# Optimization experiments

Measured on AMD Instinct MI355X. Metric: run time of the kernel, lower is better.

## Reference

```python
import jax, jax.numpy as jnp
import numpy as np

B, S, F_IN, D, H, L, E, DFF, OUT = 16, 512, 46, 256, 8, 6, 8, 1024, 3


def _ln(x, s, b, eps=1e-5):
    m = x.mean(-1, keepdims=True)
    v = ((x - m) ** 2).mean(-1, keepdims=True)
    return (x - m) / jnp.sqrt(v + eps) * s + b


def _mha(q_in, kv_in, qkv_w, qkv_b, out_w, out_b, h):
    # torch nn.MultiheadAttention (batch_first), eval mode (no dropout)
    d = q_in.shape[-1]
    dh = d // h
    wq, wk, wv = jnp.split(qkv_w, 3, axis=0)
    bq, bk, bv = jnp.split(qkv_b, 3)
    q = (q_in @ wq.T + bq).reshape(q_in.shape[0], q_in.shape[1], h, dh)
    k = (kv_in @ wk.T + bk).reshape(kv_in.shape[0], kv_in.shape[1], h, dh)
    v = (kv_in @ wv.T + bv).reshape(kv_in.shape[0], kv_in.shape[1], h, dh)
    attn = jax.nn.softmax(jnp.einsum('bqhd,bkhd->bhqk', q, k) / jnp.sqrt(jnp.float32(dh)), axis=-1)
    o = jnp.einsum('bhqk,bkhd->bqhd', attn, v).reshape(q_in.shape[0], q_in.shape[1], d)
    return o @ out_w.T + out_b


def _moe(x, gate_w, gate_b, e_w1, e_b1, e_w2, e_b2, top_k=2):
    # Faithful to source: EVERY expert runs its dense FFN over all tokens,
    # then outputs are mixed by the top-k gate weights (zero for unrouted experts).
    logits = x @ gate_w.T + gate_b                      # (B,S,E)
    tk_logits, tk_idx = jax.lax.top_k(logits, top_k)    # (B,S,K)
    tk_probs = jax.nn.softmax(tk_logits, axis=-1)
    onehot = jax.nn.one_hot(tk_idx, logits.shape[-1], dtype=x.dtype)  # (B,S,K,E)
    weights = (onehot * tk_probs[..., None]).sum(-2)    # (B,S,E)
    hid = jax.nn.gelu(jnp.einsum('bsd,efd->bsef', x, e_w1) + e_b1, approximate=False)  # (B,S,E,DFF)
    out_e = jnp.einsum('bsef,edf->bsed', hid, e_w2) + e_b2                             # (B,S,E,D)
    out = jnp.einsum('bsed,bse->bsd', out_e, weights)
    probs = jax.nn.softmax(logits, axis=-1)
    aux = logits.shape[-1] * jnp.sum(probs.mean(axis=(0, 1)) ** 2)
    return out, aux


def _posenc(s, d):
    pos = jnp.arange(s, dtype=jnp.float32)[:, None]
    div = jnp.exp(jnp.arange(0, d, 2, dtype=jnp.float32) * (-np.log(10000.0) / d))
    pe = jnp.zeros((s, d), jnp.float32)
    pe = pe.at[:, 0::2].set(jnp.sin(pos * div)).at[:, 1::2].set(jnp.cos(pos * div))
    return pe


def _forward(x, in_w, in_b, l_qkv_w, l_qkv_b, l_out_w, l_out_b, gate_w, gate_b,
             e_w1, e_b1, e_w2, e_b2, ln1_s, ln1_b, ln2_s, ln2_b,
             p_qkv_w, p_qkv_b, p_out_w, p_out_b,
             a_w1, a_b1, a_ln1s, a_ln1b, a_w2, a_b2, a_ln2s, a_ln2b, a_w3, a_b3,
             pr_w1, pr_b1, pr_ln1s, pr_ln1b, pr_w2, pr_b2, pr_ln2s, pr_ln2b, pr_w3, pr_b3):
    h = x @ in_w.T + in_b + _posenc(x.shape[1], D)[None]
    aux_total = jnp.float32(0.0)
    # NB: source builds ModuleList([encoder_layer]*L) with the SAME instance -> shared weights
    for _ in range(L):
        attn = _mha(h, h, l_qkv_w, l_qkv_b, l_out_w, l_out_b, H)
        h = _ln(h + attn, ln1_s, ln1_b)
        moe_out, aux = _moe(h, gate_w, gate_b, e_w1, e_b1, e_w2, e_b2)
        aux_total = aux_total + aux
        h = _ln(h + moe_out, ln2_s, ln2_b)
    pooled = _mha(h[:, -1:, :], h, p_qkv_w, p_qkv_b, p_out_w, p_out_b, H)[:, 0]  # (B,D)
    # action head: Linear -> GELU -> LN -> Linear -> GELU -> LN -> Linear
    a = jax.nn.gelu(pooled @ a_w1.T + a_b1, approximate=False)
    a = _ln(a, a_ln1s, a_ln1b)
    a = jax.nn.gelu(a @ a_w2.T + a_b2, approximate=False)
    a = _ln(a, a_ln2s, a_ln2b)
    action = a @ a_w3.T + a_b3
    # profit head: Linear -> LN -> GELU -> Linear -> LN -> GELU -> Linear
    p = jax.nn.gelu(_ln(pooled @ pr_w1.T + pr_b1, pr_ln1s, pr_ln1b), approximate=False)
    p = jax.nn.gelu(_ln(p @ pr_w2.T + pr_b2, pr_ln2s, pr_ln2b), approximate=False)
    profit = p @ pr_w3.T + pr_b3
    return action, profit, aux_total


def setup_inputs() -> dict:
    key = jax.random.key(0)
    ks = iter(jax.random.split(key, 64))
    def w(shape, scale=0.02):
        return jax.random.normal(next(ks), shape, jnp.float32) * scale
    d2, d4 = D // 2, D // 4
    return dict(
        x=jax.random.normal(next(ks), (B, S, F_IN), jnp.float32),
        in_w=w((D, F_IN)), in_b=jnp.zeros(D),
        l_qkv_w=w((3 * D, D)), l_qkv_b=jnp.zeros(3 * D), l_out_w=w((D, D)), l_out_b=jnp.zeros(D),
        gate_w=w((E, D)), gate_b=jnp.zeros(E),
        e_w1=w((E, DFF, D)), e_b1=jnp.zeros((E, DFF)), e_w2=w((E, D, DFF)), e_b2=jnp.zeros((E, D)),
        ln1_s=jnp.ones(D), ln1_b=jnp.zeros(D), ln2_s=jnp.ones(D), ln2_b=jnp.zeros(D),
        p_qkv_w=w((3 * D, D)), p_qkv_b=jnp.zeros(3 * D), p_out_w=w((D, D)), p_out_b=jnp.zeros(D),
        a_w1=w((d2, D)), a_b1=jnp.zeros(d2), a_ln1s=jnp.ones(d2), a_ln1b=jnp.zeros(d2),
        a_w2=w((d4, d2)), a_b2=jnp.zeros(d4), a_ln2s=jnp.ones(d4), a_ln2b=jnp.zeros(d4),
        a_w3=w((OUT, d4)), a_b3=jnp.zeros(OUT),
        pr_w1=w((D, D)), pr_b1=jnp.zeros(D), pr_ln1s=jnp.ones(D), pr_ln1b=jnp.zeros(D),
        pr_w2=w((d2, D)), pr_b2=jnp.zeros(d2), pr_ln2s=jnp.ones(d2), pr_ln2b=jnp.zeros(d2),
        pr_w3=w((1, d2)), pr_b3=jnp.zeros(1),
    )


def reference(x, in_w, in_b, l_qkv_w, l_qkv_b, l_out_w, l_out_b, gate_w, gate_b,
              e_w1, e_b1, e_w2, e_b2, ln1_s, ln1_b, ln2_s, ln2_b,
              p_qkv_w, p_qkv_b, p_out_w, p_out_b,
              a_w1, a_b1, a_ln1s, a_ln1b, a_w2, a_b2, a_ln2s, a_ln2b, a_w3, a_b3,
              pr_w1, pr_b1, pr_ln1s, pr_ln1b, pr_w2, pr_b2, pr_ln2s, pr_ln2b, pr_w3, pr_b3):
    return _forward(x, in_w, in_b, l_qkv_w, l_qkv_b, l_out_w, l_out_b, gate_w, gate_b,
                    e_w1, e_b1, e_w2, e_b2, ln1_s, ln1_b, ln2_s, ln2_b,
                    p_qkv_w, p_qkv_b, p_out_w, p_out_b,
                    a_w1, a_b1, a_ln1s, a_ln1b, a_w2, a_b2, a_ln2s, a_ln2b, a_w3, a_b3,
                    pr_w1, pr_b1, pr_ln1s, pr_ln1b, pr_w2, pr_b2, pr_ln2s, pr_ln2b, pr_w3, pr_b3)
```

## Files before the change

### kernel.cpp

```cpp
#include <hip/hip_runtime.h>
#include <hip/hip_bf16.h>
#include <math.h>


typedef __bf16 bf16;
typedef __bf16 bf16x8 __attribute__((ext_vector_type(8)));
typedef __bf16 bf16x4 __attribute__((ext_vector_type(4)));
typedef float f32x4 __attribute__((ext_vector_type(4)));

#define NIN 41

#define GLOAD_LDS(g, l)                                                    \
    __builtin_amdgcn_global_load_lds(                                      \
        (const __attribute__((address_space(1))) void*)(g),                \
        (__attribute__((address_space(3))) void*)(l), 16, 0, 0)

struct InTab {
    const void* src[NIN];
    unsigned off[NIN];
    unsigned n[NIN];
};

__device__ __forceinline__ float gelu_exact(float x) {
    return 0.5f * x * (1.0f + erff(x * 0.70710678118654752f));
}

__global__ void sniff_kernel(const unsigned* __restrict__ xw, int* __restrict__ flag) {
    __shared__ int cnt;
    if (threadIdx.x == 0) cnt = 0;
    __syncthreads();
    const unsigned w = xw[threadIdx.x];
    const unsigned ex = (w >> 7) & 0xFFu;
    if (ex >= 107u && ex <= 133u) atomicAdd(&cnt, 1);
    __syncthreads();
    if (threadIdx.x == 0) *flag = (cnt >= 192) ? 1 : 0;
}

__global__ __launch_bounds__(256) void convert_kernel(
    InTab tab, bf16* __restrict__ dst_base, const int* __restrict__ flag) {
    const unsigned g0 = blockIdx.x * 1024u;
    int inp = 0;
#pragma unroll
    for (int i = 1; i < NIN; i++)
        if (g0 >= tab.off[i]) inp = i;
    const unsigned n = tab.n[inp];
    const unsigned i0 = g0 - tab.off[inp] + threadIdx.x * 4u;
    if (i0 >= n) return;
    const int isbf = *flag;
    bf16* dst = dst_base + tab.off[inp];
    const unsigned end = (i0 + 4u > n) ? n : i0 + 4u;
    if (isbf) {
        const unsigned short* s = (const unsigned short*)tab.src[inp];
        for (unsigned i = i0; i < end; i++) ((unsigned short*)dst)[i] = s[i];
    } else {
        const float* s = (const float*)tab.src[inp];
        for (unsigned i = i0; i < end; i++) dst[i] = (bf16)s[i];
    }
}

__global__ void out_convert_kernel(const float* __restrict__ st, void* __restrict__ out,
                                   const int* __restrict__ flag) {
    const int i = threadIdx.x;
    if (i >= 65) return;
    if (*flag) ((bf16*)out)[i] = (bf16)st[i];
    else       ((float*)out)[i] = st[i];
}

#define SWZ(r, c) (((r) * 8 + ((c) ^ ((r) & 7))) * 8)

template <int BM, int BN, int WM, int WN, bool VTOUT>
__global__ __launch_bounds__(256) void gemm_bt(
    const bf16* __restrict__ A, const bf16* __restrict__ W,
    const bf16* __restrict__ bias, bf16* __restrict__ C,
    int M, int N, int K, bf16* __restrict__ vT) {
    constexpr int BK = 64;
    __shared__ alignas(16) bf16 As[BM * BK];
    __shared__ alignas(16) bf16 Ws[BN * BK];
    const int bm0 = blockIdx.x * BM, bn0 = blockIdx.y * BN;
    const int tid = threadIdx.x;
    const int wave = tid >> 6, lane = tid & 63;
    constexpr int WCOLS = BN / WN;
    const int wm0 = (wave / WCOLS) * WM, wn0 = (wave % WCOLS) * WN;
    constexpr int MT = WM / 16, NT = WN / 16;
    f32x4 acc[MT][NT] = {};
    const int frow = lane & 15, fquad = lane >> 4;

    constexpr int AIT = BM / 32, BIT = BN / 32;
    const bf16* ag[AIT];
    const bf16* bg[BIT];
    unsigned al[AIT], bl[BIT];
#pragma unroll
    for (int i = 0; i < AIT; i++) {
        const int d = wave * (BM * 2) + i * 64 + lane;
        const int r = d >> 3, c = ((d & 7) ^ (r & 7)) * 8;
        ag[i] = A + (size_t)(bm0 + r) * K + c;
        al[i] = (unsigned)(wave * (BM * 2) + i * 64) * 8u;
    }
#pragma unroll
    for (int i = 0; i < BIT; i++) {
        const int d = wave * (BN * 2) + i * 64 + lane;
        const int r = d >> 3, c = ((d & 7) ^ (r & 7)) * 8;
        bg[i] = W + (size_t)(bn0 + r) * K + c;
        bl[i] = (unsigned)(wave * (BN * 2) + i * 64) * 8u;
    }

    for (int k0 = 0; k0 < K; k0 += BK) {
#pragma unroll
        for (int i = 0; i < AIT; i++) GLOAD_LDS(ag[i] + k0, &As[al[i]]);
#pragma unroll
        for (int i = 0; i < BIT; i++) GLOAD_LDS(bg[i] + k0, &Ws[bl[i]]);
        __syncthreads();
#pragma unroll
        for (int ks = 0; ks < BK / 32; ks++) {
            bf16x8 af[MT], bfr[NT];
#pragma unroll
            for (int mt = 0; mt < MT; mt++) {
                const int r = wm0 + mt * 16 + frow;
                af[mt] = *(const bf16x8*)&As[SWZ(r, ks * 4 + fquad)];
            }
#pragma unroll
            for (int nt = 0; nt < NT; nt++) {
                const int r = wn0 + nt * 16 + frow;
                bfr[nt] = *(const bf16x8*)&Ws[SWZ(r, ks * 4 + fquad)];
            }
#pragma unroll
            for (int mt = 0; mt < MT; mt++)
#pragma unroll
                for (int nt = 0; nt < NT; nt++)
                    acc[mt][nt] = __builtin_amdgcn_mfma_f32_16x16x32_bf16(
                        af[mt], bfr[nt], acc[mt][nt], 0, 0, 0);
        }
        __syncthreads();
    }

#pragma unroll
    for (int mt = 0; mt < MT; mt++)
#pragma unroll
        for (int nt = 0; nt < NT; nt++) {
            const int gn = bn0 + wn0 + nt * 16 + frow;
            const float bv = (float)bias[gn];
#pragma unroll
            for (int r = 0; r < 4; r++) {
                const int gm = bm0 + wm0 + mt * 16 + fquad * 4 + r;
                const float v = acc[mt][nt][r] + bv;
                if (VTOUT && gn >= 512) {
                    const int d = gn - 512;
                    const int bb = gm >> 9, s = gm & 511;
                    vT[((size_t)(bb * 8 + (d >> 5)) * 32 + (d & 31)) * 512 + s] = (bf16)v;
// ... 118 lines not shown
    const bf16* bg[2];
    unsigned al[4], bl[2];
#pragma unroll
    for (int i = 0; i < 4; i++) {
        const int d = wave * 256 + i * 64 + lane;
        const int r = d >> 3, c = ((d & 7) ^ (r & 7)) * 8;
        ag[i] = A + (size_t)(bm0 + r) * K + c;
        al[i] = (unsigned)(wave * 256 + i * 64) * 8u;
    }
#pragma unroll
    for (int i = 0; i < 2; i++) {
        const int d = wave * 128 + i * 64 + lane;
        const int r = d >> 3, c = ((d & 7) ^ (r & 7)) * 8;
        bg[i] = W + (size_t)(bn0 + r) * K + c;
        bl[i] = (unsigned)(wave * 128 + i * 64) * 8u;
    }

    for (int k0 = 0; k0 < K; k0 += BK) {
#pragma unroll
        for (int i = 0; i < 4; i++) GLOAD_LDS(ag[i] + k0, &As[al[i]]);
#pragma unroll
        for (int i = 0; i < 2; i++) GLOAD_LDS(bg[i] + k0, &Ws[bl[i]]);
        __syncthreads();
#pragma unroll
        for (int ks = 0; ks < 2; ks++) {
            bf16x8 af[MT], bfr[NT];
#pragma unroll
            for (int mt = 0; mt < MT; mt++) {
                const int r = wm0 + mt * 16 + frow;
                af[mt] = *(const bf16x8*)&As[SWZ(r, ks * 4 + fquad)];
            }
#pragma unroll
            for (int nt = 0; nt < NT; nt++) {
                const int r = nt * 16 + frow;
                bfr[nt] = *(const bf16x8*)&Ws[SWZ(r, ks * 4 + fquad)];
            }
#pragma unroll
            for (int mt = 0; mt < MT; mt++)
#pragma unroll
                for (int nt = 0; nt < NT; nt++)
                    acc[mt][nt] = __builtin_amdgcn_mfma_f32_16x16x32_bf16(
                        af[mt], bfr[nt], acc[mt][nt], 0, 0, 0);
        }
        __syncthreads();
    }

#pragma unroll
    for (int mt = 0; mt < MT; mt++)
#pragma unroll
        for (int nt = 0; nt < NT; nt++) {
            const int gn = bn0 + nt * 16 + frow;
            const float bv = (float)bias[gn];
#pragma unroll
            for (int r = 0; r < 4; r++) {
                const int gm = bm0 + wm0 + mt * 16 + fquad * 4 + r;
                const float v = acc[mt][nt][r] + bv;
                C[(size_t)mylist[gm] * 256 + gn] = (bf16)(mylw[gm] * v);
            }
        }
}

__global__ __launch_bounds__(256) void input_proj_kernel(
    const bf16* __restrict__ x, const bf16* __restrict__ w,
    const bf16* __restrict__ b, bf16* __restrict__ h) {
    const int m = blockIdx.x, t = threadIdx.x;
    __shared__ float xs[46];
    if (t < 46) xs[t] = (float)x[m * 46 + t];
    __syncthreads();
    float acc = (float)b[t];
#pragma unroll
    for (int k = 0; k < 46; k++) acc += xs[k] * (float)w[t * 46 + k];
    const int s = m & 511;
    const int i = t >> 1;
    const float dv = expf((float)(2 * i) * (-9.210340371976184f / 256.0f));
    const float ang = (float)s * dv;
    const float pe = (t & 1) ? cosf(ang) : sinf(ang);
    h[(size_t)m * 256 + t] = (bf16)(acc + pe);
}

__global__ __launch_bounds__(256) void ln_kernel(
    bf16* __restrict__ h, const bf16* __restrict__ a0,
    const bf16* __restrict__ a1, const bf16* __restrict__ s,
    const bf16* __restrict__ b) {
    const int m = blockIdx.x * 4 + (threadIdx.x >> 6);
    const int lane = threadIdx.x & 63;
    const int c0 = lane * 4;
    bf16x4 hv = *(const bf16x4*)&h[(size_t)m * 256 + c0];
    bf16x4 av = *(const bf16x4*)&a0[(size_t)m * 256 + c0];
    bf16x4 bv2 = *(const bf16x4*)&a1[(size_t)m * 256 + c0];
    float x[4];
    float s1 = 0.0f, s2 = 0.0f;
#pragma unroll
    for (int j = 0; j < 4; j++) {
        x[j] = (float)hv[j] + (float)av[j] + (float)bv2[j];
        s1 += x[j];
        s2 += x[j] * x[j];
    }
#pragma unroll
    for (int msk = 1; msk < 64; msk <<= 1) {
        s1 += __shfl_xor(s1, msk, 64);
        s2 += __shfl_xor(s2, msk, 64);
    }
    const float mean = s1 * (1.0f / 256.0f);
    const float var = fmaxf(s2 * (1.0f / 256.0f) - mean * mean, 0.0f);
    const float inv = rsqrtf(var + 1e-5f);
    bf16x4 sv = *(const bf16x4*)&s[c0];
    bf16x4 bv = *(const bf16x4*)&b[c0];
    bf16x4 o;
#pragma unroll
    for (int j = 0; j < 4; j++)
        o[j] = (bf16)((x[j] - mean) * inv * (float)sv[j] + (float)bv[j]);
    *(bf16x4*)&h[(size_t)m * 256 + c0] = o;
}

__global__ __launch_bounds__(256) void gate_ln_kernel(
    bf16* __restrict__ h, const bf16* __restrict__ addv,
    const bf16* __restrict__ lns, const bf16* __restrict__ lnb,
    const bf16* __restrict__ gw, const bf16* __restrict__ gb,
    int* __restrict__ top_e, float* __restrict__ top_w,
    int* __restrict__ g_hist, float* __restrict__ aux_sums) {
    __shared__ alignas(16) bf16 hs[128][264];
    __shared__ alignas(16) bf16 gws[8][264];
    __shared__ float lg[128][9];
    __shared__ float mxs[128], invs[128];
    __shared__ int hist[16];
    const int tid = threadIdx.x;
    {
        const int e = tid >> 5, k = (tid & 31) * 8;
        *(bf16x8*)&gws[e][k] = *(const bf16x8*)&gw[e * 256 + k];
    }
    if (tid < 16) hist[tid] = 0;

    const int tl = tid >> 1, half = tid & 1;
    const int tok = blockIdx.x * 128 + tl;
    const int c0 = half * 128;
    float s1 = 0.0f, s2 = 0.0f;
#pragma unroll
    for (int j = 0; j < 128; j += 8) {
        bf16x8 hv = *(const bf16x8*)&h[(size_t)tok * 256 + c0 + j];
        bf16x8 av = *(const bf16x8*)&addv[(size_t)tok * 256 + c0 + j];
        bf16x8 xw;
#pragma unroll
        for (int q = 0; q < 8; q++) {
            const float xq = (float)hv[q] + (float)av[q];
            xw[q] = (bf16)xq;
            s1 += xq;
            s2 += xq * xq;
        }
        *(bf16x8*)&hs[tl][c0 + j] = xw;
    }
    s1 += __shfl_xor(s1, 1, 64);
    s2 += __shfl_xor(s2, 1, 64);
    const float mean = s1 * (1.0f / 256.0f);
    const float var = fmaxf(s2 * (1.0f / 256.0f) - mean * mean, 0.0f);
    const float inv = rsqrtf(var + 1e-5f);
#pragma unroll
    for (int j = 0; j < 128; j += 8) {
        bf16x8 xw = *(const bf16x8*)&hs[tl][c0 + j];
        bf16x8 sv = *(const bf16x8*)&lns[c0 + j];
        bf16x8 bv = *(const bf16x8*)&lnb[c0 + j];
        bf16x8 o;
#pragma unroll
        for (int q = 0; q < 8; q++)
            o[q] = (bf16)(((float)xw[q] - mean) * inv * (float)sv[q] + (float)bv[q]);
        *(bf16x8*)&hs[tl][c0 + j] = o;
        *(bf16x8*)&h[(size_t)tok * 256 + c0 + j] = o;
    }
    __syncthreads();

    const int e = tid & 7;
#pragma unroll
    for (int pass = 0; pass < 4; pass++) {
        const int t2 = pass * 32 + (tid >> 3);
        float acc = 0.0f;
        for (int k = 0; k < 256; k += 8) {
            bf16x8 hv = *(const bf16x8*)&hs[t2][k];
            bf16x8 wv = *(const bf16x8*)&gws[e][k];
#pragma unroll
            for (int q = 0; q < 8; q++) acc += (float)hv[q] * (float)wv[q];
        }
        lg[t2][e] = acc + (float)gb[e];
    }
    __syncthreads();

    if (tid < 128) {
        const int t2 = blockIdx.x * 128 + tid;
        float l[8];
#pragma unroll
        for (int j = 0; j < 8; j++) l[j] = lg[tid][j];
        int i0 = 0;
#pragma unroll
        for (int j = 1; j < 8; j++)
            if (l[j] > l[i0]) i0 = j;
        int i1 = -1;
#pragma unroll
        for (int j = 0; j < 8; j++)
            if (j != i0 && (i1 < 0 || l[j] > l[i1])) i1 = j;
        const float p0 = 1.0f / (1.0f + expf(l[i1] - l[i0]));
        top_e[t2] = i0;         top_w[t2] = p0;
        top_e[8192 + t2] = i1;  top_w[8192 + t2] = 1.0f - p0;
        atomicAdd(&hist[i0], 1);
        atomicAdd(&hist[8 + i1], 1);
        const float mx = l[i0];
        float se = 0.0f;
#pragma unroll
        for (int j = 0; j < 8; j++) se += expf(l[j] - mx);
        mxs[tid] = mx;
        invs[tid] = 1.0f / se;
    }
    __syncthreads();
    if (tid < 8) {
        float s = 0.0f;
        for (int t = 0; t < 128; t++) s += expf(lg[t][tid] - mxs[t]) * invs[t];
        atomicAdd(&aux_sums[tid], s);
    }
    if (tid < 16) g_hist[blockIdx.x * 16 + tid] = hist[tid];
}

__global__ __launch_bounds__(256) void scatter_route_kernel(
    const int* __restrict__ g_hist, const int* __restrict__ top_e,
    const float* __restrict__ top_w, int* __restrict__ ntiles,
    int* __restrict__ tile_ex, int* __restrict__ list, float* __restrict__ lw) {
    __shared__ int gh[64][16];
    __shared__ int s_cnt[16], s_pre[16], s_off[16], pos[16];
    const int tid = threadIdx.x;
    for (int i = tid; i < 1024; i += 256) gh[i >> 4][i & 15] = g_hist[i];
    __syncthreads();
    if (tid < 16) {
        int run = 0, pre = 0;
        for (int b = 0; b < 64; b++) {
            if (b == (int)blockIdx.x) pre = run;
            run += gh[b][tid];
        }
        s_cnt[tid] = run;
        s_pre[tid] = pre;
    }
    __syncthreads();
    if (tid < 2) {
        const int slot = tid;
        int o = 0;
        for (int e2 = 0; e2 < 8; e2++) {
            s_off[slot * 8 + e2] = o;
            const int nt = (s_cnt[slot * 8 + e2] + 127) >> 7;
            if (blockIdx.x == 0)
                for (int t = 0; t < nt; t++) tile_ex[slot * 72 + (o >> 7) + t] = e2;
            o += nt << 7;
        }
        if (blockIdx.x == 0) ntiles[slot] = o >> 7;
    }
    __syncthreads();
    if (tid < 16) pos[tid] = s_off[tid] + s_pre[tid];
    __syncthreads();
    if (blockIdx.x == 0) {
        for (int idx = tid; idx < 16 * 128; idx += 256) {
            const int seg = idx >> 7, i = idx & 127;
            const int slot = seg >> 3;
            const int start = s_off[seg] + s_cnt[seg];
            const int end = s_off[seg] + ((s_cnt[seg] + 127) & ~127);
            const int p = start + i;
            if (p < end) {
                list[slot * 9216 + p] = 8192;
                lw[slot * 9216 + p] = 0.0f;
            }
        }
    }
    if (tid < 128) {
        const int tok = blockIdx.x * 128 + tid;
#pragma unroll
        for (int slot = 0; slot < 2; slot++) {
            const int e = top_e[slot * 8192 + tok];
            const float w = top_w[slot * 8192 + tok];
            const int idx = atomicAdd(&pos[slot * 8 + e], 1);
            list[slot * 9216 + idx] = tok;
            lw[slot * 9216 + idx] = w;
        }
    }
}

__global__ __launch_bounds__(256) void attn_kernel(
    const bf16* __restrict__ qkv, const bf16* __restrict__ vT,
    bf16* __restrict__ aout) {
    __shared__ alignas(16) bf16 P[32][520];
    __shared__ float wsum[4][32];
    __shared__ float sinv[32];
    const int s0 = blockIdx.x * 32;
    const int b = blockIdx.y >> 3, hh = blockIdx.y & 7;
    const int tid = threadIdx.x, wave = tid >> 6, lane = tid & 63;
    const int frow = lane & 15, fquad = lane >> 4;
    const size_t base = (size_t)b * 512;
    const float CST = 0.25505654f;

    bf16x8 qf[2];
#pragma unroll
    for (int mt = 0; mt < 2; mt++)
        qf[mt] = *(const bf16x8*)&qkv[(base + s0 + mt * 16 + frow) * 768 + hh * 32 + fquad * 8];
    float rsum[2][4] = {};
#pragma unroll
    for (int k8 = 0; k8 < 8; k8++) {
        const int key0 = (wave * 8 + k8) * 16;
        bf16x8 kf = *(const bf16x8*)&qkv[(base + key0 + frow) * 768 + 256 + hh * 32 + fquad * 8];
#pragma unroll
        for (int mt = 0; mt < 2; mt++) {
            f32x4 c = {};
            c = __builtin_amdgcn_mfma_f32_16x16x32_bf16(qf[mt], kf, c, 0, 0, 0);
#pragma unroll
            for (int r = 0; r < 4; r++) {
                const float e_ = __builtin_exp2f(fminf(c[r] * CST, 60.0f));
                P[mt * 16 + fquad * 4 + r][key0 + frow] = (bf16)e_;
                rsum[mt][r] += e_;
            }
        }
    }
#pragma unroll
    for (int mt = 0; mt < 2; mt++)
#pragma unroll
        for (int r = 0; r < 4; r++) {
#pragma unroll
            for (int m = 1; m < 16; m <<= 1)
                rsum[mt][r] += __shfl_xor(rsum[mt][r], m, 64);
        }
    if (frow == 0) {
#pragma unroll
        for (int mt = 0; mt < 2; mt++)
#pragma unroll
            for (int r = 0; r < 4; r++)
                wsum[wave][mt * 16 + fquad * 4 + r] = rsum[mt][r];
    }
    __syncthreads();
    if (tid < 32)
        sinv[tid] = 1.0f / (wsum[0][tid] + wsum[1][tid] + wsum[2][tid] + wsum[3][tid]);

    {
        const int mt = wave >> 1, nt = wave & 1;
        const bf16* vrow = &vT[((size_t)(b * 8 + hh) * 32 + nt * 16 + frow) * 512];
        f32x4 o = {};
#pragma unroll
        for (int ks = 0; ks < 16; ks++) {
            bf16x8 pf = *(const bf16x8*)&P[mt * 16 + frow][ks * 32 + fquad * 8];
            bf16x8 vf = *(const bf16x8*)&vrow[ks * 32 + fquad * 8];
            o = __builtin_amdgcn_mfma_f32_16x16x32_bf16(pf, vf, o, 0, 0, 0);
        }
        __syncthreads();
        const int r0 = mt * 16 + fquad * 4;
#pragma unroll
        for (int r = 0; r < 4; r++)
            aout[(base + s0 + r0 + r) * 256 + hh * 32 + nt * 16 + frow] =
                (bf16)(o[r] * sinv[r0 + r]);
    }
}

__global__ __launch_bounds__(256) void pooled_attn_kernel(
    const bf16* __restrict__ qkv, const bf16* __restrict__ vT,
    bf16* __restrict__ pa) {
    const int wid = blockIdx.x * 4 + (threadIdx.x >> 6);
    const int lane = threadIdx.x & 63;
    const int b = wid >> 3, hh = wid & 7;
    const size_t base = (size_t)b * 512;
    const float scale = 0.17677669529663687f;
    float q[32];
#pragma unroll
    for (int d = 0; d < 32; d++) q[d] = (float)qkv[(base + 511) * 768 + hh * 32 + d];
    float sc[8];
    float mx = -1e30f;
#pragma unroll
    for (int j = 0; j < 8; j++) {
        const int key = lane + j * 64;
        const bf16* kr = &qkv[(base + key) * 768 + 256 + hh * 32];
        float s = 0.0f;
#pragma unroll
        for (int d = 0; d < 32; d++) s += q[d] * (float)kr[d];
        s *= scale;
        sc[j] = s;
        mx = fmaxf(mx, s);
    }
#pragma unroll
    for (int m = 1; m < 64; m <<= 1) mx = fmaxf(mx, __shfl_xor(mx, m, 64));
    float se = 0.0f;
#pragma unroll
    for (int j = 0; j < 8; j++) { sc[j] = expf(sc[j] - mx); se += sc[j]; }
#pragma unroll
    for (int m = 1; m < 64; m <<= 1) se += __shfl_xor(se, m, 64);
    float o[32] = {};
    const bf16* vb = &vT[(size_t)(b * 8 + hh) * 32 * 512];
#pragma unroll
    for (int d = 0; d < 32; d++) {
        const bf16* vr = vb + (size_t)d * 512;
#pragma unroll
        for (int j = 0; j < 8; j++)
            o[d] += sc[j] * (float)vr[lane + j * 64];
    }
#pragma unroll
    for (int d = 0; d < 32; d++) {
#pragma unroll
        for (int m = 1; m < 64; m <<= 1) o[d] += __shfl_xor(o[d], m, 64);
    }
    if (lane == 0) {
        const float inv = 1.0f / se;
        for (int d = 0; d < 32; d++) pa[b * 256 + hh * 32 + d] = (bf16)(o[d] * inv);
    }
}

__global__ __launch_bounds__(256) void pooled_proj_kernel(
    const bf16* __restrict__ pa, const bf16* __restrict__ w,
    const bf16* __restrict__ bias, bf16* __restrict__ pooled) {
    const int b = blockIdx.x, t = threadIdx.x;
    __shared__ float xs[256];
    xs[t] = (float)pa[b * 256 + t];
    __syncthreads();
    float acc = (float)bias[t];
    for (int k = 0; k < 256; k++) acc += xs[k] * (float)w[t * 256 + k];
    pooled[b * 256 + t] = (bf16)acc;
}

__global__ __launch_bounds__(256) void heads_kernel(
    const bf16* __restrict__ pooled,
    const bf16* __restrict__ aw1, const bf16* __restrict__ ab1,
    const bf16* __restrict__ aln1s, const bf16* __restrict__ aln1b,
    const bf16* __restrict__ aw2, const bf16* __restrict__ ab2,
    const bf16* __restrict__ aln2s, const bf16* __restrict__ aln2b,
    const bf16* __restrict__ aw3, const bf16* __restrict__ ab3,
    const bf16* __restrict__ pw1, const bf16* __restrict__ pb1,
    const bf16* __restrict__ pln1s, const bf16* __restrict__ pln1b,
    const bf16* __restrict__ pw2, const bf16* __restrict__ pb2,
    const bf16* __restrict__ pln2s, const bf16* __restrict__ pln2b,
    const bf16* __restrict__ pw3, const bf16* __restrict__ pb3,
    float* __restrict__ out) {
    const int b = blockIdx.x, t = threadIdx.x;
    __shared__ float pool[256], buf[256], buf2[256], r1[256], r2[256];
    pool[t] = (float)pooled[b * 256 + t];
    __syncthreads();

    auto block_ln = [&](float* v, int W, const bf16* ls, const bf16* lb) {
        const float val = (t < W) ? v[t] : 0.0f;
        r1[t] = val;
        r2[t] = val * val;
        __syncthreads();
        for (int off = 128; off > 0; off >>= 1) {
            if (t < off) { r1[t] += r1[t + off]; r2[t] += r2[t + off]; }
            __syncthreads();
        }
        const float mean = r1[0] / (float)W;
        const float var = fmaxf(r2[0] / (float)W - mean * mean, 0.0f);
        const float inv = rsqrtf(var + 1e-5f);
        __syncthreads();
        if (t < W) v[t] = (val - mean) * inv * (float)ls[t] + (float)lb[t];
        __syncthreads();
    };

    float a;
    if (t < 128) {
        a = (float)ab1[t];
        for (int k = 0; k < 256; k++) a += pool[k] * (float)aw1[t * 256 + k];
        buf[t] = gelu_exact(a);
    }
    __syncthreads();
    block_ln(buf, 128, aln1s, aln1b);
    if (t < 64) {
        a = (float)ab2[t];
        for (int k = 0; k < 128; k++) a += buf[k] * (float)aw2[t * 128 + k];
        buf2[t] = gelu_exact(a);
    }
    __syncthreads();
    block_ln(buf2, 64, aln2s, aln2b);
    if (t < 3) {
        a = (float)ab3[t];
        for (int k = 0; k < 64; k++) a += buf2[k] * (float)aw3[t * 64 + k];
        out[b * 3 + t] = a;
    }

    a = (float)pb1[t];
    for (int k = 0; k < 256; k++) a += pool[k] * (float)pw1[t * 256 + k];
    buf[t] = a;
    __syncthreads();
    block_ln(buf, 256, pln1s, pln1b);
    buf[t] = gelu_exact(buf[t]);
    __syncthreads();
    if (t < 128) {
        a = (float)pb2[t];
        for (int k = 0; k < 256; k++) a += buf[k] * (float)pw2[t * 256 + k];
        buf2[t] = a;
    }
    __syncthreads();
    block_ln(buf2, 128, pln2s, pln2b);
    if (t < 128) buf2[t] = gelu_exact(buf2[t]);
    __syncthreads();
    if (t == 0) {
        a = (float)pb3[0];
        for (int k = 0; k < 128; k++) a += buf2[k] * (float)pw3[k];
        out[48 + b] = a;
    }
}

__global__ void aux_kernel(const float* __restrict__ sums, float* __restrict__ out) {
    if (threadIdx.x == 0 && blockIdx.x == 0) {
        float tot = 0.0f;
        for (int l = 0; l < 6; l++)
            for (int e = 0; e < 8; e++) {
                const float mn = sums[l * 8 + e] * (1.0f / 8192.0f);
                tot += 8.0f * mn * mn;
            }
        out[64] = tot;
    }
}

extern "C" void kernel_launch(void* const* d_in, const int* in_sizes, int n_in,
                              void* d_out, int out_size, void* d_ws, size_t ws_size,
                              hipStream_t stream) {
    char* ws = (char*)d_ws;
    const size_t MB = 1024 * 1024;
    bf16*  h     = (bf16*)(ws);
    bf16*  moe0  = (bf16*)(ws + 8 * MB);
    bf16*  moe1  = (bf16*)(ws + 13 * MB);
    char*  ctrl  = ws + 20 * MB;
    float* auxs   = (float*)(ctrl + 0);
    int*   flag   = (int*)(ctrl + 192);
    int*   ntiles = (int*)(ctrl + 256);
    int*   tileex = (int*)(ctrl + 320);
    float* ostage = (float*)(ctrl + 1024);
    int*   g_hist = (int*)(ctrl + 2048);
    int*   top_e  = (int*)(ctrl + 10240);
    float* top_w  = (float*)(ctrl + 75776);
    int*   list   = (int*)(ctrl + 141312);
    float* lw     = (float*)(ctrl + 215040);
    bf16*  qkv   = (bf16*)(ws + 24 * MB);
    bf16*  aoutb = (bf16*)(ws + 40 * MB);
    bf16*  projo = (bf16*)(ws + 48 * MB);
    bf16*  hid0  = (bf16*)(ws + 56 * MB);
    bf16*  hid1  = (bf16*)(ws + 80 * MB);
    bf16*  vT    = (bf16*)(ws + 104 * MB);
    bf16*  pattn  = (bf16*)(ws + 110 * MB);
    bf16*  pooled = (bf16*)(ws + 110 * MB + 8192);
    bf16*  cvbase = (bf16*)(ws + 112 * MB);

    InTab tab;
    unsigned off = 0;
    bf16* cv[NIN];
    for (int i = 0; i < NIN; i++) {
        tab.src[i] = d_in[i];
        tab.off[i] = off;
        tab.n[i] = (unsigned)in_sizes[i];
        cv[i] = cvbase + off;
        off += ((unsigned)in_sizes[i] + 1023u) & ~1023u;
    }
    const int cv_blocks = (int)(off >> 10);

    const bf16 *x = cv[0], *in_w = cv[1], *in_b = cv[2], *qkv_w = cv[3], *qkv_b = cv[4],
               *out_w = cv[5], *out_b = cv[6], *gate_w = cv[7], *gate_b = cv[8],
               *e_w1 = cv[9], *e_b1 = cv[10], *e_w2 = cv[11], *e_b2 = cv[12],
               *ln1_s = cv[13], *ln1_b = cv[14], *ln2_s = cv[15], *ln2_b = cv[16],
               *pqkv_w = cv[17], *pqkv_b = cv[18], *pout_w = cv[19], *pout_b = cv[20],
               *a_w1 = cv[21], *a_b1 = cv[22], *a_ln1s = cv[23], *a_ln1b = cv[24],
               *a_w2 = cv[25], *a_b2 = cv[26], *a_ln2s = cv[27], *a_ln2b = cv[28],
               *a_w3 = cv[29], *a_b3 = cv[30],
               *pr_w1 = cv[31], *pr_b1 = cv[32], *pr_ln1s = cv[33], *pr_ln1b = cv[34],
               *pr_w2 = cv[35], *pr_b2 = cv[36], *pr_ln2s = cv[37], *pr_ln2b = cv[38],
               *pr_w3 = cv[39], *pr_b3 = cv[40];

    sniff_kernel<<<1, 256, 0, stream>>>((const unsigned*)d_in[0], flag);
    convert_kernel<<<cv_blocks, 256, 0, stream>>>(tab, cvbase, flag);

    hipMemsetAsync(auxs, 0, 192, stream);
    input_proj_kernel<<<8192, 256, 0, stream>>>(x, in_w, in_b, h);

    for (int l = 0; l < 6; l++) {
        gemm_bt<64, 128, 32, 64, true><<<dim3(128, 6), 256, 0, stream>>>(
            h, qkv_w, qkv_b, qkv, 8192, 768, 256, vT);
        attn_kernel<<<dim3(16, 128), 256, 0, stream>>>(qkv, vT, aoutb);
        gemm_bt<64, 64, 32, 32, false><<<dim3(128, 4), 256, 0, stream>>>(
            aoutb, out_w, out_b, projo, 8192, 256, 256, vT);
        gate_ln_kernel<<<64, 256, 0, stream>>>(h, projo, ln1_s, ln1_b,
                                               gate_w, gate_b,
                                               top_e, top_w, g_hist, auxs + l * 8);
        scatter_route_kernel<<<64, 256, 0, stream>>>(g_hist, top_e, top_w,
                                                     ntiles, tileex, list, lw);
        gemm_moe_w1<<<dim3(142, 8), 256, 0, stream>>>(
            h, e_w1, e_b1, hid0, hid1, list, tileex, ntiles);
        gemm_moe_w2<<<dim3(142, 4), 256, 0, stream>>>(
            hid0, hid1, e_w2, e_b2, moe0, moe1, list, lw, tileex, ntiles);
        ln_kernel<<<2048, 256, 0, stream>>>(h, moe0, moe1, ln2_s, ln2_b);
    }

    gemm_bt<64, 128, 32, 64, true><<<dim3(128, 6), 256, 0, stream>>>(
        h, pqkv_w, pqkv_b, qkv, 8192, 768, 256, vT);
    pooled_attn_kernel<<<32, 256, 0, stream>>>(qkv, vT, pattn);
    pooled_proj_kernel<<<16, 256, 0, stream>>>(pattn, pout_w, pout_b, pooled);

    heads_kernel<<<16, 256, 0, stream>>>(
        pooled,
        a_w1, a_b1, a_ln1s, a_ln1b, a_w2, a_b2, a_ln2s, a_ln2b, a_w3, a_b3,
        pr_w1, pr_b1, pr_ln1s, pr_ln1b, pr_w2, pr_b2, pr_ln2s, pr_ln2b, pr_w3, pr_b3,
        ostage);
    aux_kernel<<<1, 64, 0, stream>>>(auxs, ostage);
    out_convert_kernel<<<1, 128, 0, stream>>>(ostage, d_out, flag);
}
```

Baseline: 1.090 ms.

## Fuse attention out-projection with residual LN and gating; merge pooled and head kernels

Replaces the separate out-projection GEMM and gate/LN kernel with a single kernel that does the projection, residual add, LayerNorm, gate logits, top-2 routing and aux sums for 32-row tiles. This removes the projo round trip and a launch per layer. The pooled attention, pooled projection and head MLPs become one 512-thread kernel, and the aux reduction moves into the output conversion kernel. The routing prefix scan is adapted to the larger number of histogram blocks, and the second LN kernel is widened to 8-element vectors.

After: 1.010 ms. -7.4%, faster.

```diff
diff --git a/kernel.cpp b/kernel.cpp
--- a/kernel.cpp
+++ b/kernel.cpp
@@ -58,12 +58,26 @@
     }
 }
 
-__global__ void out_convert_kernel(const float* __restrict__ st, void* __restrict__ out,
+__global__ void out_convert_kernel(const float* __restrict__ st,
+                                   const float* __restrict__ auxsums,
+                                   void* __restrict__ out,
                                    const int* __restrict__ flag) {
     const int i = threadIdx.x;
     if (i >= 65) return;
-    if (*flag) ((bf16*)out)[i] = (bf16)st[i];
-    else       ((float*)out)[i] = st[i];
+    float v;
+    if (i == 64) {
+        float tot = 0.0f;
+        for (int l = 0; l < 6; l++)
+            for (int e = 0; e < 8; e++) {
+                const float mn = auxsums[l * 8 + e] * (1.0f / 8192.0f);
+                tot += 8.0f * mn * mn;
+            }
+        v = tot;
+    } else {
+        v = st[i];
+    }
+    if (*flag) ((bf16*)out)[i] = (bf16)v;
+    else       ((float*)out)[i] = v;
 }
 
 #define SWZ(r, c) (((r) * 8 + ((c) ^ ((r) & 7))) * 8)
@@ -348,112 +362,209 @@
     bf16* __restrict__ h, const bf16* __restrict__ a0,
     const bf16* __restrict__ a1, const bf16* __restrict__ s,
     const bf16* __restrict__ b) {
-    const int m = blockIdx.x * 4 + (threadIdx.x >> 6);
-    const int lane = threadIdx.x & 63;
-    const int c0 = lane * 4;
-    bf16x4 hv = *(const bf16x4*)&h[(size_t)m * 256 + c0];
-    bf16x4 av = *(const bf16x4*)&a0[(size_t)m * 256 + c0];
-    bf16x4 bv2 = *(const bf16x4*)&a1[(size_t)m * 256 + c0];
-    float x[4];
+    const int wv = threadIdx.x >> 6, lane = threadIdx.x & 63;
+    const int m = blockIdx.x * 8 + wv * 2 + (lane >> 5);
+    const int c0 = (lane & 31) * 8;
+    const size_t off = (size_t)m * 256 + c0;
+    bf16x8 hv = *(const bf16x8*)&h[off];
+    bf16x8 av = *(const bf16x8*)&a0[off];
+    bf16x8 bv2 = *(const bf16x8*)&a1[off];
+    float x[8];
     float s1 = 0.0f, s2 = 0.0f;
 #pragma unroll
-    for (int j = 0; j < 4; j++) {
+    for (int j = 0; j < 8; j++) {
         x[j] = (float)hv[j] + (float)av[j] + (float)bv2[j];
         s1 += x[j];
         s2 += x[j] * x[j];
     }
 #pragma unroll
-    for (int msk = 1; msk < 64; msk <<= 1) {
+    for (int msk = 1; msk < 32; msk <<= 1) {
         s1 += __shfl_xor(s1, msk, 64);
         s2 += __shfl_xor(s2, msk, 64);
     }
     const float mean = s1 * (1.0f / 256.0f);
     const float var = fmaxf(s2 * (1.0f / 256.0f) - mean * mean, 0.0f);
     const float inv = rsqrtf(var + 1e-5f);
-    bf16x4 sv = *(const bf16x4*)&s[c0];
-    bf16x4 bv = *(const bf16x4*)&b[c0];
-    bf16x4 o;
-#pragma unroll
-    for (int j = 0; j < 4; j++)
+    bf16x8 sv = *(const bf16x8*)&s[c0];
+    bf16x8 bv = *(const bf16x8*)&b[c0];
+    bf16x8 o;
+#pragma unroll
+    for (int j = 0; j < 8; j++)
         o[j] = (bf16)((x[j] - mean) * inv * (float)sv[j] + (float)bv[j]);
-    *(bf16x4*)&h[(size_t)m * 256 + c0] = o;
-}
-
-__global__ __launch_bounds__(256) void gate_ln_kernel(
-    bf16* __restrict__ h, const bf16* __restrict__ addv,
+    *(bf16x8*)&h[off] = o;
+}
+
+__global__ __launch_bounds__(256) void proj_gate_ln_kernel(
+    const bf16* __restrict__ A, const bf16* __restrict__ W,
+    const bf16* __restrict__ bias, bf16* __restrict__ h,
     const bf16* __restrict__ lns, const bf16* __restrict__ lnb,
     const bf16* __restrict__ gw, const bf16* __restrict__ gb,
     int* __restrict__ top_e, float* __restrict__ top_w,
     int* __restrict__ g_hist, float* __restrict__ aux_sums) {
-    __shared__ alignas(16) bf16 hs[128][264];
-    __shared__ alignas(16) bf16 gws[8][264];
-    __shared__ float lg[128][9];
-    __shared__ float mxs[128], invs[128];
-    __shared__ int hist[16];
+    __shared__ alignas(16) bf16 As[32 * 64];
+    __shared__ alignas(16) bf16 Ws[256 * 64];
+    __shared__ alignas(16) bf16 hs[32 * 264];
+    __shared__ alignas(16) bf16 gws[8 * 264];
+    __shared__ float rws1[4][32], rws2[4][32];
+    __shared__ float meanv[32], invv[32];
+    __shared__ float lg[256];
+    __shared__ int sh_hist[16];
+    __shared__ float sh_aux[8];
+
+    const int bm0 = blockIdx.x * 32;
     const int tid = threadIdx.x;
+    const int wave = tid >> 6, lane = tid & 63;
+    const int wn0 = (wave & 3) * 64;
+    const int frow = lane & 15, fquad = lane >> 4;
+    f32x4 acc[2][4] = {};
+
+    const int da = wave * 64 + lane;
+    const int ra = da >> 3, ca = ((da & 7) ^ (ra & 7)) * 8;
+    const bf16* ag = A + (size_t)(bm0 + ra) * 256 + ca;
+    const unsigned al = (unsigned)(wave * 64) * 8u;
+    const bf16* bg[8];
+    unsigned bl[8];
+#pragma unroll
+    for (int i = 0; i < 8; i++) {
+        const int d = wave * 512 + i * 64 + lane;
+        const int r = d >> 3, c = ((d & 7) ^ (r & 7)) * 8;
+        bg[i] = W + (size_t)r * 256 + c;
+        bl[i] = (unsigned)(wave * 512 + i * 64) * 8u;
+    }
+
+    {
+        const int rr = tid >> 3, ccb = (tid & 7) * 32;
+        const bf16* src = &h[(size_t)(bm0 + rr) * 256 + ccb];
+        bf16x8 v0 = *(const bf16x8*)&src[0];
+        bf16x8 v1 = *(const bf16x8*)&src[8];
+        bf16x8 v2 = *(const bf16x8*)&src[16];
+        bf16x8 v3 = *(const bf16x8*)&src[24];
+        bf16* dst = &hs[rr * 264 + ccb];
+        *(bf16x8*)&dst[0] = v0;
+        *(bf16x8*)&dst[8] = v1;
+        *(bf16x8*)&dst[16] = v2;
+        *(bf16x8*)&dst[24] = v3;
+    }
     {
         const int e = tid >> 5, k = (tid & 31) * 8;
-        *(bf16x8*)&gws[e][k] = *(const bf16x8*)&gw[e * 256 + k];
-    }
-    if (tid < 16) hist[tid] = 0;
-
-    const int tl = tid >> 1, half = tid & 1;
-    const int tok = blockIdx.x * 128 + tl;
-    const int c0 = half * 128;
-    float s1 = 0.0f, s2 = 0.0f;
-#pragma unroll
-    for (int j = 0; j < 128; j += 8) {
-        bf16x8 hv = *(const bf16x8*)&h[(size_t)tok * 256 + c0 + j];
-        bf16x8 av = *(const bf16x8*)&addv[(size_t)tok * 256 + c0 + j];
-        bf16x8 xw;
-#pragma unroll
-        for (int q = 0; q < 8; q++) {
-            const float xq = (float)hv[q] + (float)av[q];
-            xw[q] = (bf16)xq;
-            s1 += xq;
-            s2 += xq * xq;
-        }
-        *(bf16x8*)&hs[tl][c0 + j] = xw;
-    }
-    s1 += __shfl_xor(s1, 1, 64);
-    s2 += __shfl_xor(s2, 1, 64);
-    const float mean = s1 * (1.0f / 256.0f);
-    const float var = fmaxf(s2 * (1.0f / 256.0f) - mean * mean, 0.0f);
-    const float inv = rsqrtf(var + 1e-5f);
-#pragma unroll
-    for (int j = 0; j < 128; j += 8) {
-        bf16x8 xw = *(const bf16x8*)&hs[tl][c0 + j];
-        bf16x8 sv = *(const bf16x8*)&lns[c0 + j];
-        bf16x8 bv = *(const bf16x8*)&lnb[c0 + j];
-        bf16x8 o;
-#pragma unroll
-        for (int q = 0; q < 8; q++)
-            o[q] = (bf16)(((float)xw[q] - mean) * inv * (float)sv[q] + (float)bv[q]);
-        *(bf16x8*)&hs[tl][c0 + j] = o;
-        *(bf16x8*)&h[(size_t)tok * 256 + c0 + j] = o;
-    }
-    __syncthreads();
-
-    const int e = tid & 7;
-#pragma unroll
-    for (int pass = 0; pass < 4; pass++) {
-        const int t2 = pass * 32 + (tid >> 3);
-        float acc = 0.0f;
+        *(bf16x8*)&gws[e * 264 + k] = *(const bf16x8*)&gw[e * 256 + k];
+    }
+    if (tid < 16) sh_hist[tid] = 0;
+    if (tid < 8) sh_aux[tid] = 0.0f;
+
+    for (int k0 = 0; k0 < 256; k0 += 64) {
+        GLOAD_LDS(ag + k0, &As[al]);
+#pragma unroll
+        for (int i = 0; i < 8; i++) GLOAD_LDS(bg[i] + k0, &Ws[bl[i]]);
+        __syncthreads();
+#pragma unroll
+        for (int ks = 0; ks < 2; ks++) {
+            bf16x8 af[2], bfr[4];
+#pragma unroll
+            for (int mt = 0; mt < 2; mt++)
+                af[mt] = *(const bf16x8*)&As[SWZ(mt * 16 + frow, ks * 4 + fquad)];
+#pragma unroll
+            for (int nt = 0; nt < 4; nt++)
+                bfr[nt] = *(const bf16x8*)&Ws[SWZ(wn0 + nt * 16 + frow, ks * 4 + fquad)];
+#pragma unroll
+            for (int mt = 0; mt < 2; mt++)
+#pragma unroll
+                for (int nt = 0; nt < 4; nt++)
+                    acc[mt][nt] = __builtin_amdgcn_mfma_f32_16x16x32_bf16(
+                        af[mt], bfr[nt], acc[mt][nt], 0, 0, 0);
+        }
+        __syncthreads();
+    }
+
+    float s1v[2][4] = {}, s2v[2][4] = {};
+#pragma unroll
+    for (int mt = 0; mt < 2; mt++)
+#pragma unroll
+        for (int nt = 0; nt < 4; nt++) {
+            const int gn = wn0 + nt * 16 + frow;
+            const float bv = (float)bias[gn];
+#pragma unroll
+            for (int r = 0; r < 4; r++) {
+                const int row = mt * 16 + fquad * 4 + r;
+                const float x = acc[mt][nt][r] + bv + (float)hs[row * 264 + gn];
+                acc[mt][nt][r] = x;
+                s1v[mt][r] += x;
+                s2v[mt][r] += x * x;
+            }
+        }
+#pragma unroll
+    for (int mt = 0; mt < 2; mt++)
+#pragma unroll
+        for (int r = 0; r < 4; r++) {
+#pragma unroll
+            for (int m = 1; m < 16; m <<= 1) {
+                s1v[mt][r] += __shfl_xor(s1v[mt][r], m, 64);
+                s2v[mt][r] += __shfl_xor(s2v[mt][r], m, 64);
+            }
+        }
+    if (frow == 0) {
+#pragma unroll
+        for (int mt = 0; mt < 2; mt++)
+#pragma unroll
+            for (int r = 0; r < 4; r++) {
+                const int row = mt * 16 + fquad * 4 + r;
+                rws1[wave][row] = s1v[mt][r];
+                rws2[wave][row] = s2v[mt][r];
+            }
+    }
+    __syncthreads();
+    if (tid < 32) {
+        const float a = rws1[0][tid] + rws1[1][tid] + rws1[2][tid] + rws1[3][tid];
+        const float c2 = rws2[0][tid] + rws2[1][tid] + rws2[2][tid] + rws2[3][tid];
+        const float mean = a * (1.0f / 256.0f);
+        const float var = fmaxf(c2 * (1.0f / 256.0f) - mean * mean, 0.0f);
+        meanv[tid] = mean;
+        invv[tid] = rsqrtf(var + 1e-5f);
+    }
+    __syncthreads();
+
+#pragma unroll
+    for (int mt = 0; mt < 2; mt++)
+#pragma unroll
+        for (int nt = 0; nt < 4; nt++) {
+            const int gn = wn0 + nt * 16 + frow;
+            const float sg = (float)lns[gn], bgn = (float)lnb[gn];
+#pragma unroll
+            for (int r = 0; r < 4; r++) {
+                const int row = mt * 16 + fquad * 4 + r;
+                const float o = (acc[mt][nt][r] - meanv[row]) * invv[row] * sg + bgn;
+                hs[row * 264 + gn] = (bf16)o;
+            }
+        }
+    __syncthreads();
+
+    {
+        const int rr = tid >> 3, ccb = (tid & 7) * 32;
+        bf16* dst = &h[(size_t)(bm0 + rr) * 256 + ccb];
+        const bf16* src = &hs[rr * 264 + ccb];
+        *(bf16x8*)&dst[0] = *(const bf16x8*)&src[0];
+        *(bf16x8*)&dst[8] = *(const bf16x8*)&src[8];
+        *(bf16x8*)&dst[16] = *(const bf16x8*)&src[16];
+        *(bf16x8*)&dst[24] = *(const bf16x8*)&src[24];
+    }
+    {
+        const int row = tid >> 3, e = tid & 7;
+        float acg = (float)gb[e];
         for (int k = 0; k < 256; k += 8) {
-            bf16x8 hv = *(const bf16x8*)&hs[t2][k];
-            bf16x8 wv = *(const bf16x8*)&gws[e][k];
-#pragma unroll
-            for (int q = 0; q < 8; q++) acc += (float)hv[q] * (float)wv[q];
-        }
-        lg[t2][e] = acc + (float)gb[e];
-    }
-    __syncthreads();
-
-    if (tid < 128) {
-        const int t2 = blockIdx.x * 128 + tid;
+            bf16x8 hv = *(const bf16x8*)&hs[row * 264 + k];
+            bf16x8 wv = *(const bf16x8*)&gws[e * 264 + k];
+#pragma unroll
+            for (int q = 0; q < 8; q++) acg += (float)hv[q] * (float)wv[q];
+        }
+        lg[row * 8 + e] = acg;
+    }
+    __syncthreads();
+
+    if (tid < 32) {
+        const int tok = bm0 + tid;
         float l[8];
 #pragma unroll
-        for (int j = 0; j < 8; j++) l[j] = lg[tid][j];
+        for (int j = 0; j < 8; j++) l[j] = lg[tid * 8 + j];
         int i0 = 0;
 #pragma unroll
         for (int j = 1; j < 8; j++)
@@ -463,41 +574,47 @@
         for (int j = 0; j < 8; j++)
             if (j != i0 && (i1 < 0 || l[j] > l[i1])) i1 = j;
         const float p0 = 1.0f / (1.0f + expf(l[i1] - l[i0]));
-        top_e[t2] = i0;         top_w[t2] = p0;
-        top_e[8192 + t2] = i1;  top_w[8192 + t2] = 1.0f - p0;
-        atomicAdd(&hist[i0], 1);
-        atomicAdd(&hist[8 + i1], 1);
+        top_e[tok] = i0;         top_w[tok] = p0;
+        top_e[8192 + tok] = i1;  top_w[8192 + tok] = 1.0f - p0;
+        atomicAdd(&sh_hist[i0], 1);
+        atomicAdd(&sh_hist[8 + i1], 1);
         const float mx = l[i0];
         float se = 0.0f;
 #pragma unroll
-        for (int j = 0; j < 8; j++) se += expf(l[j] - mx);
-        mxs[tid] = mx;
-        invs[tid] = 1.0f / se;
-    }
-    __syncthreads();
-    if (tid < 8) {
-        float s = 0.0f;
-        for (int t = 0; t < 128; t++) s += expf(lg[t][tid] - mxs[t]) * invs[t];
-        atomicAdd(&aux_sums[tid], s);
-    }
-    if (tid < 16) g_hist[blockIdx.x * 16 + tid] = hist[tid];
+        for (int j = 0; j < 8; j++) { l[j] = expf(l[j] - mx); se += l[j]; }
+        const float si = 1.0f / se;
+#pragma unroll
+        for (int j = 0; j < 8; j++) atomicAdd(&sh_aux[j], l[j] * si);
+    }
+    __syncthreads();
+    if (tid < 16) g_hist[blockIdx.x * 16 + tid] = sh_hist[tid];
+    if (tid < 8) atomicAdd(&aux_sums[tid], sh_aux[tid]);
 }
 
 __global__ __launch_bounds__(256) void scatter_route_kernel(
     const int* __restrict__ g_hist, const int* __restrict__ top_e,
     const float* __restrict__ top_w, int* __restrict__ ntiles,
     int* __restrict__ tile_ex, int* __restrict__ list, float* __restrict__ lw) {
-    __shared__ int gh[64][16];
+    __shared__ int gh[256][16];
+    __shared__ int ps[16][8];
     __shared__ int s_cnt[16], s_pre[16], s_off[16], pos[16];
     const int tid = threadIdx.x;
-    for (int i = tid; i < 1024; i += 256) gh[i >> 4][i & 15] = g_hist[i];
+    for (int i = tid; i < 4096; i += 256) gh[i >> 4][i & 15] = g_hist[i];
+    __syncthreads();
+    if (tid < 128) {
+        const int se = tid >> 3, ch = tid & 7;
+        int s = 0;
+        for (int b = ch * 32; b < ch * 32 + 32; b++) s += gh[b][se];
+        ps[se][ch] = s;
+    }
     __syncthreads();
     if (tid < 16) {
-        int run = 0, pre = 0;
-        for (int b = 0; b < 64; b++) {
-            if (b == (int)blockIdx.x) pre = run;
-            run += gh[b][tid];
-        }
+        int run = 0;
+        for (int ch = 0; ch < 8; ch++) run += ps[tid][ch];
+        const int b0 = (int)blockIdx.x * 4;
+        int pre = 0;
+        for (int ch = 0; ch < (b0 >> 5); ch++) pre += ps[tid][ch];
+        for (int b = b0 & ~31; b < b0; b++) pre += gh[b][tid];
         s_cnt[tid] = run;
         s_pre[tid] = pre;
     }
@@ -615,71 +732,9 @@
     }
 }
 
-__global__ __launch_bounds__(256) void pooled_attn_kernel(
+__global__ __launch_bounds__(512) void pooled_heads_kernel(
     const bf16* __restrict__ qkv, const bf16* __restrict__ vT,
-    bf16* __restrict__ pa) {
-    const int wid = blockIdx.x * 4 + (threadIdx.x >> 6);
-    const int lane = threadIdx.x & 63;
-    const int b = wid >> 3, hh = wid & 7;
-    const size_t base = (size_t)b * 512;
-    const float scale = 0.17677669529663687f;
-    float q[32];
-#pragma unroll
-    for (int d = 0; d < 32; d++) q[d] = (float)qkv[(base + 511) * 768 + hh * 32 + d];
-    float sc[8];
-    float mx = -1e30f;
-#pragma unroll
-    for (int j = 0; j < 8; j++) {
-        const int key = lane + j * 64;
-        const bf16* kr = &qkv[(base + key) * 768 + 256 + hh * 32];
-        float s = 0.0f;
-#pragma unroll
-        for (int d = 0; d < 32; d++) s += q[d] * (float)kr[d];
-        s *= scale;
-        sc[j] = s;
-        mx = fmaxf(mx, s);
-    }
-#pragma unroll
-    for (int m = 1; m < 64; m <<= 1) mx = fmaxf(mx, __shfl_xor(mx, m, 64));
-    float se = 0.0f;
-#pragma unroll
-    for (int j = 0; j < 8; j++) { sc[j] = expf(sc[j] - mx); se += sc[j]; }
-#pragma unroll
-    for (int m = 1; m < 64; m <<= 1) se += __shfl_xor(se, m, 64);
-    float o[32] = {};
-    const bf16* vb = &vT[(size_t)(b * 8 + hh) * 32 * 512];
-#pragma unroll
-    for (int d = 0; d < 32; d++) {
-        const bf16* vr = vb + (size_t)d * 512;
-#pragma unroll
-        for (int j = 0; j < 8; j++)
-            o[d] += sc[j] * (float)vr[lane + j * 64];
-    }
-#pragma unroll
-    for (int d = 0; d < 32; d++) {
-#pragma unroll
-        for (int m = 1; m < 64; m <<= 1) o[d] += __shfl_xor(o[d], m, 64);
-    }
-    if (lane == 0) {
-        const float inv = 1.0f / se;
-        for (int d = 0; d < 32; d++) pa[b * 256 + hh * 32 + d] = (bf16)(o[d] * inv);
-    }
-}
-
-__global__ __launch_bounds__(256) void pooled_proj_kernel(
-    const bf16* __restrict__ pa, const bf16* __restrict__ w,
-    const bf16* __restrict__ bias, bf16* __restrict__ pooled) {
-    const int b = blockIdx.x, t = threadIdx.x;
-    __shared__ float xs[256];
-    xs[t] = (float)pa[b * 256 + t];
-    __syncthreads();
-    float acc = (float)bias[t];
-    for (int k = 0; k < 256; k++) acc += xs[k] * (float)w[t * 256 + k];
-    pooled[b * 256 + t] = (bf16)acc;
-}
-
-__global__ __launch_bounds__(256) void heads_kernel(
-    const bf16* __restrict__ pooled,
+    const bf16* __restrict__ pout_w, const bf16* __restrict__ pout_b,
     const bf16* __restrict__ aw1, const bf16* __restrict__ ab1,
     const bf16* __restrict__ aln1s, const bf16* __restrict__ aln1b,
     const bf16* __restrict__ aw2, const bf16* __restrict__ ab2,
@@ -692,14 +747,71 @@
     const bf16* __restrict__ pw3, const bf16* __restrict__ pb3,
     float* __restrict__ out) {
     const int b = blockIdx.x, t = threadIdx.x;
+    __shared__ float pa_s[256];
     __shared__ float pool[256], buf[256], buf2[256], r1[256], r2[256];
-    pool[t] = (float)pooled[b * 256 + t];
+
+    {
+        const int hh = t >> 6, lane = t & 63;
+        const size_t base = (size_t)b * 512;
+        const float scale = 0.17677669529663687f;
+        float q[32];
+#pragma unroll
+        for (int d = 0; d < 32; d++) q[d] = (float)qkv[(base + 511) * 768 + hh * 32 + d];
+        float sc[8];
+        float mx = -1e30f;
+#pragma unroll
+        for (int j = 0; j < 8; j++) {
+            const int key = lane + j * 64;
+            const bf16* kr = &qkv[(base + key) * 768 + 256 + hh * 32];
+            float s = 0.0f;
+#pragma unroll
+            for (int d = 0; d < 32; d++) s += q[d] * (float)kr[d];
+            s *= scale;
+            sc[j] = s;
+            mx = fmaxf(mx, s);
+        }
+#pragma unroll
+        for (int m = 1; m < 64; m <<= 1) mx = fmaxf(mx, __shfl_xor(mx, m, 64));
+        float se = 0.0f;
+#pragma unroll
+        for (int j = 0; j < 8; j++) { sc[j] = expf(sc[j] - mx); se += sc[j]; }
+#pragma unroll
+        for (int m = 1; m < 64; m <<= 1) se += __shfl_xor(se, m, 64);
+        float o[32] = {};
+        const bf16* vb = &vT[(size_t)(b * 8 + hh) * 32 * 512];
+#pragma unroll
+        for (int d = 0; d < 32; d++) {
+            const bf16* vr = vb + (size_t)d * 512;
+#pragma unroll
+            for (int j = 0; j < 8; j++)
+                o[d] += sc[j] * (float)vr[lane + j * 64];
+        }
+#pragma unroll
+        for (int d = 0; d < 32; d++) {
+#pragma unroll
+            for (int m = 1; m < 64; m <<= 1) o[d] += __shfl_xor(o[d], m, 64);
+        }
+        if (lane == 0) {
+            const float inv = 1.0f / se;
+            for (int d = 0; d < 32; d++) pa_s[hh * 32 + d] = o[d] * inv;
+        }
+    }
+    __syncthreads();
+
+    if (t < 256) {
+        float a = (float)pout_b[t];
+        for (int k = 0; k < 256; k++) a += pa_s[k] * (float)pout_w[t * 256 + k];
+        pool[t] = a;
+    }
     __syncthreads();
 
     auto block_ln = [&](float* v, int W, const bf16* ls, const bf16* lb) {
-        const float val = (t < W) ? v[t] : 0.0f;
-        r1[t] = val;
-        r2[t] = val * val;
+        float val = 0.0f;
+        if (t < 256) {
+            val = (t < W) ? v[t] : 0.0f;
+            r1[t] = val;
+            r2[t] = val * val;
+        }
         __syncthreads();
         for (int off = 128; off > 0; off >>= 1) {
             if (t < off) { r1[t] += r1[t + off]; r2[t] += r2[t + off]; }
@@ -713,36 +825,37 @@
         __syncthreads();
     };
 
-    float a;
     if (t < 128) {
-        a = (float)ab1[t];
+        float a = (float)ab1[t];
         for (int k = 0; k < 256; k++) a += pool[k] * (float)aw1[t * 256 + k];
         buf[t] = gelu_exact(a);
     }
     __syncthreads();
     block_ln(buf, 128, aln1s, aln1b);
     if (t < 64) {
-        a = (float)ab2[t];
+        float a = (float)ab2[t];
         for (int k = 0; k < 128; k++) a += buf[k] * (float)aw2[t * 128 + k];
         buf2[t] = gelu_exact(a);
     }
     __syncthreads();
     block_ln(buf2, 64, aln2s, aln2b);
     if (t < 3) {
-        a = (float)ab3[t];
+        float a = (float)ab3[t];
         for (int k = 0; k < 64; k++) a += buf2[k] * (float)aw3[t * 64 + k];
         out[b * 3 + t] = a;
     }
 
-    a = (float)pb1[t];
-    for (int k = 0; k < 256; k++) a += pool[k] * (float)pw1[t * 256 + k];
-    buf[t] = a;
+    if (t < 256) {
+        float a = (float)pb1[t];
+        for (int k = 0; k < 256; k++) a += pool[k] * (float)pw1[t * 256 + k];
+        buf[t] = a;
+    }
     __syncthreads();
     block_ln(buf, 256, pln1s, pln1b);
-    buf[t] = gelu_exact(buf[t]);
+    if (t < 256) buf[t] = gelu_exact(buf[t]);
     __syncthreads();
     if (t < 128) {
-        a = (float)pb2[t];
+        float a = (float)pb2[t];
         for (int k = 0; k < 256; k++) a += buf[k] * (float)pw2[t * 256 + k];
         buf2[t] = a;
     }
@@ -751,21 +864,9 @@
     if (t < 128) buf2[t] = gelu_exact(buf2[t]);
     __syncthreads();
     if (t == 0) {
-        a = (float)pb3[0];
+        float a = (float)pb3[0];
         for (int k = 0; k < 128; k++) a += buf2[k] * (float)pw3[k];
         out[48 + b] = a;
-    }
-}
-
-__global__ void aux_kernel(const float* __restrict__ sums, float* __restrict__ out) {
-    if (threadIdx.x == 0 && blockIdx.x == 0) {
-        float tot = 0.0f;
-        for (int l = 0; l < 6; l++)
-            for (int e = 0; e < 8; e++) {
-                const float mn = sums[l * 8 + e] * (1.0f / 8192.0f);
-                tot += 8.0f * mn * mn;
-            }
-        out[64] = tot;
     }
 }
 
@@ -784,18 +885,15 @@
     int*   tileex = (int*)(ctrl + 320);
     float* ostage = (float*)(ctrl + 1024);
     int*   g_hist = (int*)(ctrl + 2048);
-    int*   top_e  = (int*)(ctrl + 10240);
-    float* top_w  = (float*)(ctrl + 75776);
-    int*   list   = (int*)(ctrl + 141312);
-    float* lw     = (float*)(ctrl + 215040);
+    int*   top_e  = (int*)(ctrl + 20480);
+    float* top_w  = (float*)(ctrl + 86016);
+    int*   list   = (int*)(ctrl + 151552);
+    float* lw     = (float*)(ctrl + 225280);
     bf16*  qkv   = (bf16*)(ws + 24 * MB);
     bf16*  aoutb = (bf16*)(ws + 40 * MB);
-    bf16*  projo = (bf16*)(ws + 48 * MB);
     bf16*  hid0  = (bf16*)(ws + 56 * MB);
     bf16*  hid1  = (bf16*)(ws + 80 * MB);
     bf16*  vT    = (bf16*)(ws + 104 * MB);
-    bf16*  pattn  = (bf16*)(ws + 110 * MB);
-    bf16*  pooled = (bf16*)(ws + 110 * MB + 8192);
     bf16*  cvbase = (bf16*)(ws + 112 * MB);
 
     InTab tab;
@@ -832,30 +930,24 @@
         gemm_bt<64, 128, 32, 64, true><<<dim3(128, 6), 256, 0, stream>>>(
             h, qkv_w, qkv_b, qkv, 8192, 768, 256, vT);
         attn_kernel<<<dim3(16, 128), 256, 0, stream>>>(qkv, vT, aoutb);
-        gemm_bt<64, 64, 32, 32, false><<<dim3(128, 4), 256, 0, stream>>>(
-            aoutb, out_w, out_b, projo, 8192, 256, 256, vT);
-        gate_ln_kernel<<<64, 256, 0, stream>>>(h, projo, ln1_s, ln1_b,
-                                               gate_w, gate_b,
-                                               top_e, top_w, g_hist, auxs + l * 8);
+        proj_gate_ln_kernel<<<256, 256, 0, stream>>>(
+            aoutb, out_w, out_b, h, ln1_s, ln1_b, gate_w, gate_b,
+            top_e, top_w, g_hist, auxs + l * 8);
         scatter_route_kernel<<<64, 256, 0, stream>>>(g_hist, top_e, top_w,
                                                      ntiles, tileex, list, lw);
         gemm_moe_w1<<<dim3(142, 8), 256, 0, stream>>>(
             h, e_w1, e_b1, hid0, hid1, list, tileex, ntiles);
         gemm_moe_w2<<<dim3(142, 4), 256, 0, stream>>>(
             hid0, hid1, e_w2, e_b2, moe0, moe1, list, lw, tileex, ntiles);
-        ln_kernel<<<2048, 256, 0, stream>>>(h, moe0, moe1, ln2_s, ln2_b);
+        ln_kernel<<<1024, 256, 0, stream>>>(h, moe0, moe1, ln2_s, ln2_b);
     }
 
     gemm_bt<64, 128, 32, 64, true><<<dim3(128, 6), 256, 0, stream>>>(
         h, pqkv_w, pqkv_b, qkv, 8192, 768, 256, vT);
-    pooled_attn_kernel<<<32, 256, 0, stream>>>(qkv, vT, pattn);
-    pooled_proj_kernel<<<16, 256, 0, stream>>>(pattn, pout_w, pout_b, pooled);
-
-    heads_kernel<<<16, 256, 0, stream>>>(
-        pooled,
+    pooled_heads_kernel<<<16, 512, 0, stream>>>(
+        qkv, vT, pout_w, pout_b,
         a_w1, a_b1, a_ln1s, a_ln1b, a_w2, a_b2, a_ln2s, a_ln2b, a_w3, a_b3,
         pr_w1, pr_b1, pr_ln1s, pr_ln1b, pr_w2, pr_b2, pr_ln2s, pr_ln2b, pr_w3, pr_b3,
         ostage);
-    aux_kernel<<<1, 64, 0, stream>>>(auxs, ostage);
-    out_convert_kernel<<<1, 128, 0, stream>>>(ostage, d_out, flag);
-}
+    out_convert_kernel<<<1, 128, 0, stream>>>(ostage, auxs, d_out, flag);
+}
```
